# Kernel optimization log

Measured on AMD Instinct MI355X. Metric: run time of the kernel, lower is better.

The kernel has to match this reference:

```python
import jax, jax.numpy as jnp
import numpy as np
import math

N = 4096
BATCH = 8192


def _bitrev_perm(n):
    stages = int(math.log2(n))
    idx = np.arange(n, dtype=np.int64)
    rev = np.zeros(n, dtype=np.int64)
    v = idx.copy()
    for _ in range(stages):
        rev = (rev << 1) | (v & 1)
        v >>= 1
    return rev


def setup_inputs() -> dict:
    key = jax.random.key(0)
    k1, k2 = jax.random.split(key)
    x_re = jax.random.normal(k1, (BATCH, N), dtype=jnp.float32)
    x_im = jax.random.normal(k2, (BATCH, N), dtype=jnp.float32)
    k = np.arange(N, dtype=np.float32)
    angles = -2.0 * np.pi * k / N
    W_re = jnp.asarray(np.cos(angles), dtype=jnp.float32)
    W_im = jnp.asarray(np.sin(angles), dtype=jnp.float32)
    bitrev = jnp.asarray(_bitrev_perm(N))
    return {"x_re": x_re, "x_im": x_im, "W_re": W_re, "W_im": W_im, "bitrev": bitrev}


def reference(x_re, x_im, W_re, W_im, bitrev):
    n = x_re.shape[-1]
    num_stages = int(math.log2(n))
    # bit-reversal input permutation (the "wiring")
    y_re = x_re[..., bitrev]
    y_im = x_im[..., bitrev]
    for stage in range(num_stages):
        stride = 1 << stage
        group_size = stride << 1
        num_groups = n // group_size
        # (..., num_groups, group_size)
        y_re = y_re.reshape(*y_re.shape[:-1], num_groups, group_size)
        y_im = y_im.reshape(*y_im.shape[:-1], num_groups, group_size)
        upper_re = y_re[..., :stride]
        upper_im = y_im[..., :stride]
        lower_re = y_re[..., stride:]
        lower_im = y_im[..., stride:]
        tw_step = n // group_size
        tw_idx = jnp.arange(stride) * tw_step
        Wr = W_re[tw_idx]
        Wi = W_im[tw_idx]
        # complex twiddle multiply: W * lower
        wb_re = Wr * lower_re - Wi * lower_im
        wb_im = Wr * lower_im + Wi * lower_re
        y_re = jnp.concatenate([upper_re + wb_re, upper_re - wb_re], axis=-1)
        y_im = jnp.concatenate([upper_im + wb_im, upper_im - wb_im], axis=-1)
        y_re = y_re.reshape(*y_re.shape[:-2], n)
        y_im = y_im.reshape(*y_im.shape[:-2], n)
    return (y_re, y_im)
```

## Files before the change

kernel.cpp:

```cpp
#include <hip/hip_runtime.h>

#define FFT_N   4096
#define THREADS 512

__device__ __forceinline__ float2 cmul(float2 w, float2 v) {
    return make_float2(fmaf(w.x, v.x, -w.y * v.y), fmaf(w.x, v.y, w.y * v.x));
}
__device__ __forceinline__ float2 cmni(float2 v) { return make_float2(v.y, -v.x); }
__device__ __forceinline__ void bfly(float2& a, float2& b, float2 w) {
    float2 t = cmul(w, b);
    b = make_float2(a.x - t.x, a.y - t.y);
    a = make_float2(a.x + t.x, a.y + t.y);
}
__device__ __forceinline__ int swz(int i) { return i ^ ((i >> 4) & 15) ^ ((i >> 8) & 15); }

__device__ __forceinline__ void bar() {
    asm volatile("s_waitcnt lgkmcnt(0)" ::: "memory");
    __builtin_amdgcn_s_barrier();
}

__device__ __forceinline__ void radix8(float2 u[8], float2 A, float2 B, float2 C, float2 D) {
    bfly(u[0], u[1], A); bfly(u[2], u[3], A); bfly(u[4], u[5], A); bfly(u[6], u[7], A);
    float2 Bn = cmni(B);
    bfly(u[0], u[2], B); bfly(u[1], u[3], Bn); bfly(u[4], u[6], B); bfly(u[5], u[7], Bn);
    float2 Cn = cmni(C), Dn = cmni(D);
    bfly(u[0], u[4], C); bfly(u[1], u[5], D); bfly(u[2], u[6], Cn); bfly(u[3], u[7], Dn);
}

__device__ __forceinline__ void load_row(float2 u[8], const float* __restrict__ xr,
                                         const float* __restrict__ xi, int t) {
    u[0] = make_float2(xr[t],        xi[t]);
    u[1] = make_float2(xr[t + 2048], xi[t + 2048]);
    u[2] = make_float2(xr[t + 1024], xi[t + 1024]);
    u[3] = make_float2(xr[t + 3072], xi[t + 3072]);
    u[4] = make_float2(xr[t + 512],  xi[t + 512]);
    u[5] = make_float2(xr[t + 2560], xi[t + 2560]);
    u[6] = make_float2(xr[t + 1536], xi[t + 1536]);
    u[7] = make_float2(xr[t + 3584], xi[t + 3584]);
}

__device__ __forceinline__ void process_row(float2 u[8], float2* lds, int t,
        float2 C1, float2 C2, float2 C3, float2 w512,
        float* __restrict__ yr, float* __restrict__ yi)
{
    const float2 one = make_float2(1.f, 0.f);
    radix8(u, one, one, one, w512);
    const int g0 = (int)(__brev((unsigned)t) >> 23);
#pragma unroll
    for (int j = 0; j < 8; ++j) lds[swz(8 * g0 + j)] = u[j];
    bar();

    const int b1 = (t & 7) | (((t >> 4) & 1) << 6) | (((t >> 3) & 1) << 7) | ((t >> 5) << 8);
#pragma unroll
    for (int j = 0; j < 8; ++j) u[j] = lds[swz(b1 + 8 * j)];
    {
        float2 B = cmul(C1, C1), A = cmul(B, B), D = cmul(C1, w512);
        radix8(u, A, B, C1, D);
    }
#pragma unroll
    for (int j = 0; j < 8; ++j) lds[swz(b1 + 8 * j)] = u[j];
    bar();

    const int b2 = (t & 63) | ((t >> 6) << 9);
#pragma unroll
    for (int j = 0; j < 8; ++j) u[j] = lds[swz(b2 + 64 * j)];
    {
        float2 B = cmul(C2, C2), A = cmul(B, B), D = cmul(C2, w512);
        radix8(u, A, B, C2, D);
    }
#pragma unroll
    for (int j = 0; j < 8; ++j) lds[swz(b2 + 64 * j)] = u[j];
    bar();

#pragma unroll
    for (int j = 0; j < 8; ++j) u[j] = lds[swz(t + 512 * j)];
    {
        float2 B = cmul(C3, C3), A = cmul(B, B), D = cmul(C3, w512);
        radix8(u, A, B, C3, D);
    }
#pragma unroll
    for (int j = 0; j < 8; ++j) { yr[t + 512 * j] = u[j].x; yi[t + 512 * j] = u[j].y; }
    bar();
}

__global__ __launch_bounds__(THREADS) void fft4096_pipe_kernel(
    const float* __restrict__ x_re, const float* __restrict__ x_im,
    const float* __restrict__ W_re, const float* __restrict__ W_im,
    float* __restrict__ out, int batch, int rows_per)
{
    __shared__ float2 lds[FFT_N];
    const int t = threadIdx.x;

    const float2 C1 = make_float2(W_re[(t & 7) << 6],  W_im[(t & 7) << 6]);
    const float2 C2 = make_float2(W_re[(t & 63) << 3], W_im[(t & 63) << 3]);
    const float2 C3 = make_float2(W_re[t],             W_im[t]);
    const float2 w512 = make_float2(0.70710678118654752f, -0.70710678118654752f);

    const int row0 = blockIdx.x * rows_per;
    float2 ua[8], ub[8];

    if (rows_per & 1) {
        for (int i = 0; i < rows_per; ++i) {
            const int r = row0 + i;
            load_row(ua, x_re + (size_t)r * FFT_N, x_im + (size_t)r * FFT_N, t);
            process_row(ua, lds, t, C1, C2, C3, w512,
                        out + (size_t)r * FFT_N, out + ((size_t)batch + r) * FFT_N);
        }
        return;
    }

    load_row(ua, x_re + (size_t)row0 * FFT_N, x_im + (size_t)row0 * FFT_N, t);
    for (int i = 0; i < rows_per; i += 2) {
        const int ra = row0 + i, rb = ra + 1;
        load_row(ub, x_re + (size_t)rb * FFT_N, x_im + (size_t)rb * FFT_N, t);
        process_row(ua, lds, t, C1, C2, C3, w512,
                    out + (size_t)ra * FFT_N, out + ((size_t)batch + ra) * FFT_N);
        if (i + 2 < rows_per) {
            const int rc = ra + 2;
            load_row(ua, x_re + (size_t)rc * FFT_N, x_im + (size_t)rc * FFT_N, t);
        }
        process_row(ub, lds, t, C1, C2, C3, w512,
                    out + (size_t)rb * FFT_N, out + ((size_t)batch + rb) * FFT_N);
    }
}

extern "C" void kernel_launch(void* const* d_in, const int* in_sizes, int n_in,
                              void* d_out, int out_size, void* d_ws, size_t ws_size,
                              hipStream_t stream) {
    const float* x_re = (const float*)d_in[0];
    const float* x_im = (const float*)d_in[1];
    const float* W_re = (const float*)d_in[2];
    const float* W_im = (const float*)d_in[3];
    const int batch = in_sizes[0] / FFT_N;
    float* out = (float*)d_out;

    int rows_per = 8;
    while (rows_per > 1 && (batch % rows_per)) rows_per >>= 1;
    const int grid = batch / rows_per;
    fft4096_pipe_kernel<<<grid, THREADS, 0, stream>>>(x_re, x_im, W_re, W_im, out, batch, rows_per);
}
```

Baseline: 112.8 us.

## Halve threads and process two interleaved sub-FFTs per thread with float4 LDS

Each thread now handles 16 complex points, two interleaved columns, instead of 8. This halves the block to 256 threads, lets global loads and stores be float2-vectorized, and packs LDS traffic into float4 with a new XOR swizzle. Output stores use nontemporal hints. The goal is fewer memory instructions and wider accesses, in exchange for higher register pressure, which the launch_bounds occupancy hint of 4 blocks tries to contain.

```diff
diff --git a/kernel.cpp b/kernel.cpp
--- a/kernel.cpp
+++ b/kernel.cpp
@@ -1,7 +1,7 @@
 #include <hip/hip_runtime.h>
 
 #define FFT_N   4096
-#define THREADS 512
+#define THREADS 256
 
 __device__ __forceinline__ float2 cmul(float2 w, float2 v) {
     return make_float2(fmaf(w.x, v.x, -w.y * v.y), fmaf(w.x, v.y, w.y * v.x));
@@ -12,13 +12,13 @@
     b = make_float2(a.x - t.x, a.y - t.y);
     a = make_float2(a.x + t.x, a.y + t.y);
 }
-__device__ __forceinline__ int swz(int i) { return i ^ ((i >> 4) & 15) ^ ((i >> 8) & 15); }
-
+__device__ __forceinline__ int sslot(int p) {
+    return p ^ ((p >> 3) & 7) ^ ((p >> 6) & 7) ^ ((p >> 9) & 7);
+}
 __device__ __forceinline__ void bar() {
     asm volatile("s_waitcnt lgkmcnt(0)" ::: "memory");
     __builtin_amdgcn_s_barrier();
 }
-
 __device__ __forceinline__ void radix8(float2 u[8], float2 A, float2 B, float2 C, float2 D) {
     bfly(u[0], u[1], A); bfly(u[2], u[3], A); bfly(u[4], u[5], A); bfly(u[6], u[7], A);
     float2 Bn = cmni(B);
@@ -27,100 +27,131 @@
     bfly(u[0], u[4], C); bfly(u[1], u[5], D); bfly(u[2], u[6], Cn); bfly(u[3], u[7], Dn);
 }
 
-__device__ __forceinline__ void load_row(float2 u[8], const float* __restrict__ xr,
-                                         const float* __restrict__ xi, int t) {
-    u[0] = make_float2(xr[t],        xi[t]);
-    u[1] = make_float2(xr[t + 2048], xi[t + 2048]);
-    u[2] = make_float2(xr[t + 1024], xi[t + 1024]);
-    u[3] = make_float2(xr[t + 3072], xi[t + 3072]);
-    u[4] = make_float2(xr[t + 512],  xi[t + 512]);
-    u[5] = make_float2(xr[t + 2560], xi[t + 2560]);
-    u[6] = make_float2(xr[t + 1536], xi[t + 1536]);
-    u[7] = make_float2(xr[t + 3584], xi[t + 3584]);
+__device__ __forceinline__ void nt_store_f2(float* p, float2 v) {
+    union { float2 f; unsigned long long u; } cv; cv.f = v;
+    __builtin_nontemporal_store(cv.u, (unsigned long long*)p);
 }
 
-__device__ __forceinline__ void process_row(float2 u[8], float2* lds, int t,
-        float2 C1, float2 C2, float2 C3, float2 w512,
+struct RowBuf { float2 re[8]; float2 im[8]; };
+
+__device__ __forceinline__ void load_row(RowBuf& rb, const float* __restrict__ xr,
+                                         const float* __restrict__ xi, int t2) {
+    const int off[8] = {0, 2048, 1024, 3072, 512, 2560, 1536, 3584};
+#pragma unroll
+    for (int j = 0; j < 8; ++j) {
+        rb.re[j] = *(const float2*)(xr + t2 + off[j]);
+        rb.im[j] = *(const float2*)(xi + t2 + off[j]);
+    }
+}
+
+__device__ __forceinline__ void process_row(const RowBuf& rb, float4* lds, int t,
+        float2 C1, float2 C2, float2 C3u, float2 C3v,
         float* __restrict__ yr, float* __restrict__ yi)
 {
-    const float2 one = make_float2(1.f, 0.f);
+    const float2 one  = make_float2(1.f, 0.f);
+    const float2 w512 = make_float2(0.70710678118654752f, -0.70710678118654752f);
+    float2 u[8], v[8];
+
+#pragma unroll
+    for (int j = 0; j < 8; ++j) {
+        u[j] = make_float2(rb.re[j].x, rb.im[j].x);
+        v[j] = make_float2(rb.re[j].y, rb.im[j].y);
+    }
     radix8(u, one, one, one, w512);
-    const int g0 = (int)(__brev((unsigned)t) >> 23);
+    radix8(v, one, one, one, w512);
+    const int g = (int)(__brev((unsigned)t) >> 24);
 #pragma unroll
-    for (int j = 0; j < 8; ++j) lds[swz(8 * g0 + j)] = u[j];
+    for (int j = 0; j < 8; ++j)
+        lds[sslot(8 * g + j)] = make_float4(u[j].x, u[j].y, v[j].x, v[j].y);
     bar();
 
-    const int b1 = (t & 7) | (((t >> 4) & 1) << 6) | (((t >> 3) & 1) << 7) | ((t >> 5) << 8);
+    const int a1 = (t & 7) | ((t >> 3) << 6);
 #pragma unroll
-    for (int j = 0; j < 8; ++j) u[j] = lds[swz(b1 + 8 * j)];
-    {
-        float2 B = cmul(C1, C1), A = cmul(B, B), D = cmul(C1, w512);
-        radix8(u, A, B, C1, D);
+    for (int j = 0; j < 8; ++j) {
+        float4 f = lds[sslot(a1 + 8 * j)];
+        u[j] = make_float2(f.x, f.y); v[j] = make_float2(f.z, f.w);
     }
+    { float2 B = cmul(C1, C1), A = cmul(B, B), D = cmul(C1, w512);
+      radix8(u, A, B, C1, D); radix8(v, A, B, C1, D); }
 #pragma unroll
-    for (int j = 0; j < 8; ++j) lds[swz(b1 + 8 * j)] = u[j];
+    for (int j = 0; j < 8; ++j)
+        lds[sslot(a1 + 8 * j)] = make_float4(u[j].x, u[j].y, v[j].x, v[j].y);
     bar();
 
-    const int b2 = (t & 63) | ((t >> 6) << 9);
+    const int a2 = (t & 63) | ((t >> 6) << 9);
 #pragma unroll
-    for (int j = 0; j < 8; ++j) u[j] = lds[swz(b2 + 64 * j)];
-    {
-        float2 B = cmul(C2, C2), A = cmul(B, B), D = cmul(C2, w512);
-        radix8(u, A, B, C2, D);
+    for (int j = 0; j < 8; ++j) {
+        float4 f = lds[sslot(a2 + 64 * j)];
+        u[j] = make_float2(f.x, f.y); v[j] = make_float2(f.z, f.w);
     }
+    { float2 B = cmul(C2, C2), A = cmul(B, B), D = cmul(C2, w512);
+      radix8(u, A, B, C2, D); radix8(v, A, B, C2, D); }
 #pragma unroll
-    for (int j = 0; j < 8; ++j) lds[swz(b2 + 64 * j)] = u[j];
+    for (int j = 0; j < 8; ++j)
+        lds[sslot(a2 + 64 * j)] = make_float4(u[j].x, u[j].y, v[j].x, v[j].y);
     bar();
 
+    const int c = 2 * t;
 #pragma unroll
-    for (int j = 0; j < 8; ++j) u[j] = lds[swz(t + 512 * j)];
-    {
-        float2 B = cmul(C3, C3), A = cmul(B, B), D = cmul(C3, w512);
-        radix8(u, A, B, C3, D);
+    for (int j = 0; j < 4; ++j) {
+        float4 f0 = lds[sslot(c + 512 * j)];
+        float4 f1 = lds[sslot(c + 1 + 512 * j)];
+        u[j] = make_float2(f0.x, f0.y); u[j + 4] = make_float2(f0.z, f0.w);
+        v[j] = make_float2(f1.x, f1.y); v[j + 4] = make_float2(f1.z, f1.w);
     }
+    { float2 B = cmul(C3u, C3u), A = cmul(B, B), D = cmul(C3u, w512);
+      radix8(u, A, B, C3u, D); }
+    { float2 B = cmul(C3v, C3v), A = cmul(B, B), D = cmul(C3v, w512);
+      radix8(v, A, B, C3v, D); }
 #pragma unroll
-    for (int j = 0; j < 8; ++j) { yr[t + 512 * j] = u[j].x; yi[t + 512 * j] = u[j].y; }
+    for (int j = 0; j < 8; ++j) {
+        nt_store_f2(yr + c + 512 * j, make_float2(u[j].x, v[j].x));
+        nt_store_f2(yi + c + 512 * j, make_float2(u[j].y, v[j].y));
+    }
     bar();
 }
 
-__global__ __launch_bounds__(THREADS) void fft4096_pipe_kernel(
+__global__ __launch_bounds__(THREADS, 4) void fft4096_p2_kernel(
     const float* __restrict__ x_re, const float* __restrict__ x_im,
     const float* __restrict__ W_re, const float* __restrict__ W_im,
     float* __restrict__ out, int batch, int rows_per)
 {
-    __shared__ float2 lds[FFT_N];
+    __shared__ float4 lds[FFT_N / 2];
     const int t = threadIdx.x;
 
     const float2 C1 = make_float2(W_re[(t & 7) << 6],  W_im[(t & 7) << 6]);
     const float2 C2 = make_float2(W_re[(t & 63) << 3], W_im[(t & 63) << 3]);
-    const float2 C3 = make_float2(W_re[t],             W_im[t]);
-    const float2 w512 = make_float2(0.70710678118654752f, -0.70710678118654752f);
+    const float2 wr2 = ((const float2*)W_re)[t];
+    const float2 wi2 = ((const float2*)W_im)[t];
+    const float2 C3u = make_float2(wr2.x, wi2.x);
+    const float2 C3v = make_float2(wr2.y, wi2.y);
 
+    const int t2 = 2 * t;
     const int row0 = blockIdx.x * rows_per;
-    float2 ua[8], ub[8];
+    RowBuf ra, rb;
 
     if (rows_per & 1) {
         for (int i = 0; i < rows_per; ++i) {
             const int r = row0 + i;
-            load_row(ua, x_re + (size_t)r * FFT_N, x_im + (size_t)r * FFT_N, t);
-            process_row(ua, lds, t, C1, C2, C3, w512,
+            load_row(ra, x_re + (size_t)r * FFT_N, x_im + (size_t)r * FFT_N, t2);
+            process_row(ra, lds, t, C1, C2, C3u, C3v,
                         out + (size_t)r * FFT_N, out + ((size_t)batch + r) * FFT_N);
         }
         return;
     }
 
-    load_row(ua, x_re + (size_t)row0 * FFT_N, x_im + (size_t)row0 * FFT_N, t);
+    load_row(ra, x_re + (size_t)row0 * FFT_N, x_im + (size_t)row0 * FFT_N, t2);
     for (int i = 0; i < rows_per; i += 2) {
-        const int ra = row0 + i, rb = ra + 1;
-        load_row(ub, x_re + (size_t)rb * FFT_N, x_im + (size_t)rb * FFT_N, t);
-        process_row(ua, lds, t, C1, C2, C3, w512,
-                    out + (size_t)ra * FFT_N, out + ((size_t)batch + ra) * FFT_N);
+        const int r0 = row0 + i, r1 = r0 + 1;
+        load_row(rb, x_re + (size_t)r1 * FFT_N, x_im + (size_t)r1 * FFT_N, t2);
+        process_row(ra, lds, t, C1, C2, C3u, C3v,
+                    out + (size_t)r0 * FFT_N, out + ((size_t)batch + r0) * FFT_N);
         if (i + 2 < rows_per) {
-            const int rc = ra + 2;
-            load_row(ua, x_re + (size_t)rc * FFT_N, x_im + (size_t)rc * FFT_N, t);
+            const int r2 = r0 + 2;
+            load_row(ra, x_re + (size_t)r2 * FFT_N, x_im + (size_t)r2 * FFT_N, t2);
         }
-        process_row(ub, lds, t, C1, C2, C3, w512,
-                    out + (size_t)rb * FFT_N, out + ((size_t)batch + rb) * FFT_N);
+        process_row(rb, lds, t, C1, C2, C3u, C3v,
+                    out + (size_t)r1 * FFT_N, out + ((size_t)batch + r1) * FFT_N);
     }
 }
 
@@ -137,5 +168,5 @@
     int rows_per = 8;
     while (rows_per > 1 && (batch % rows_per)) rows_per >>= 1;
     const int grid = batch / rows_per;
-    fft4096_pipe_kernel<<<grid, THREADS, 0, stream>>>(x_re, x_im, W_re, W_im, out, batch, rows_per);
+    fft4096_p2_kernel<<<grid, THREADS, 0, stream>>>(x_re, x_im, W_re, W_im, out, batch, rows_per);
 }
```

New measurement: 329.6 us. 192% more time.

## Switch 4096-point FFT from four radix-8 passes to three radix-16 passes

Applied to the files above, without the earlier changes.

Replaces the four radix-8 stages, which need three LDS exchanges and barriers, with three radix-16 stages that need two exchanges, using 256 threads holding 16 elements each. The first stage uses specialized trivial-twiddle butterflies. The explicit two-row register double-buffering of global loads is dropped in favour of a simple per-row loop. This cuts LDS traffic and barriers but raises register pressure and lowers threads per block, which may hurt latency hiding.

```diff
diff --git a/kernel.cpp b/kernel.cpp
--- a/kernel.cpp
+++ b/kernel.cpp
@@ -1,7 +1,7 @@
 #include <hip/hip_runtime.h>
 
 #define FFT_N   4096
-#define THREADS 512
+#define THREADS 256
 
 __device__ __forceinline__ float2 cmul(float2 w, float2 v) {
     return make_float2(fmaf(w.x, v.x, -w.y * v.y), fmaf(w.x, v.y, w.y * v.x));
@@ -12,78 +12,79 @@
     b = make_float2(a.x - t.x, a.y - t.y);
     a = make_float2(a.x + t.x, a.y + t.y);
 }
+__device__ __forceinline__ void bfly1(float2& a, float2& b) {
+    float2 t = b;
+    b = make_float2(a.x - t.x, a.y - t.y);
+    a = make_float2(a.x + t.x, a.y + t.y);
+}
+__device__ __forceinline__ void bflyni(float2& a, float2& b) {
+    float2 t = make_float2(b.y, -b.x);
+    b = make_float2(a.x - t.x, a.y - t.y);
+    a = make_float2(a.x + t.x, a.y + t.y);
+}
 __device__ __forceinline__ int swz(int i) { return i ^ ((i >> 4) & 15) ^ ((i >> 8) & 15); }
-
 __device__ __forceinline__ void bar() {
     asm volatile("s_waitcnt lgkmcnt(0)" ::: "memory");
     __builtin_amdgcn_s_barrier();
 }
 
-__device__ __forceinline__ void radix8(float2 u[8], float2 A, float2 B, float2 C, float2 D) {
-    bfly(u[0], u[1], A); bfly(u[2], u[3], A); bfly(u[4], u[5], A); bfly(u[6], u[7], A);
-    float2 Bn = cmni(B);
-    bfly(u[0], u[2], B); bfly(u[1], u[3], Bn); bfly(u[4], u[6], B); bfly(u[5], u[7], Bn);
-    float2 Cn = cmni(C), Dn = cmni(D);
-    bfly(u[0], u[4], C); bfly(u[1], u[5], D); bfly(u[2], u[6], Cn); bfly(u[3], u[7], Dn);
+#define Q1x  0.70710678118654752f
+#define Q3x -0.70710678118654752f
+#define E1x 0.923879532511286756f
+#define E1y -0.382683432365089772f
+#define E3x 0.382683432365089772f
+#define E3y -0.923879532511286756f
+
+__device__ __forceinline__ void radix16(float2 u[16], float2 G, float2 G2, float2 G4, float2 G8) {
+#pragma unroll
+    for (int m = 0; m < 16; m += 2) bfly(u[m], u[m + 1], G8);
+    float2 G4n = cmni(G4);
+#pragma unroll
+    for (int b = 0; b < 16; b += 4) { bfly(u[b], u[b + 2], G4); bfly(u[b + 1], u[b + 3], G4n); }
+    float2 t1 = cmul(G2, make_float2(Q1x, -Q1x));
+    float2 t2 = cmni(G2);
+    float2 t3 = cmul(G2, make_float2(Q3x, -Q1x));
+#pragma unroll
+    for (int b = 0; b < 16; b += 8) {
+        bfly(u[b + 0], u[b + 4], G2); bfly(u[b + 1], u[b + 5], t1);
+        bfly(u[b + 2], u[b + 6], t2); bfly(u[b + 3], u[b + 7], t3);
+    }
+    float2 s1 = cmul(G, make_float2(E1x, E1y));
+    float2 s2 = cmul(G, make_float2(Q1x, -Q1x));
+    float2 s3 = cmul(G, make_float2(E3x, E3y));
+    float2 s4 = cmni(G);
+    float2 s5 = cmni(s1);
+    float2 s6 = cmni(s2);
+    float2 s7 = cmni(s3);
+    bfly(u[0], u[8],  G);  bfly(u[1], u[9],  s1);
+    bfly(u[2], u[10], s2); bfly(u[3], u[11], s3);
+    bfly(u[4], u[12], s4); bfly(u[5], u[13], s5);
+    bfly(u[6], u[14], s6); bfly(u[7], u[15], s7);
 }
 
-__device__ __forceinline__ void load_row(float2 u[8], const float* __restrict__ xr,
-                                         const float* __restrict__ xi, int t) {
-    u[0] = make_float2(xr[t],        xi[t]);
-    u[1] = make_float2(xr[t + 2048], xi[t + 2048]);
-    u[2] = make_float2(xr[t + 1024], xi[t + 1024]);
-    u[3] = make_float2(xr[t + 3072], xi[t + 3072]);
-    u[4] = make_float2(xr[t + 512],  xi[t + 512]);
-    u[5] = make_float2(xr[t + 2560], xi[t + 2560]);
-    u[6] = make_float2(xr[t + 1536], xi[t + 1536]);
-    u[7] = make_float2(xr[t + 3584], xi[t + 3584]);
+__device__ __forceinline__ void radix16_first(float2 u[16]) {
+#pragma unroll
+    for (int m = 0; m < 16; m += 2) bfly1(u[m], u[m + 1]);
+#pragma unroll
+    for (int b = 0; b < 16; b += 4) { bfly1(u[b], u[b + 2]); bflyni(u[b + 1], u[b + 3]); }
+#pragma unroll
+    for (int b = 0; b < 16; b += 8) {
+        bfly1(u[b + 0], u[b + 4]);
+        bfly(u[b + 1], u[b + 5], make_float2(Q1x, -Q1x));
+        bflyni(u[b + 2], u[b + 6]);
+        bfly(u[b + 3], u[b + 7], make_float2(Q3x, -Q1x));
+    }
+    bfly1(u[0], u[8]);
+    bfly(u[1], u[9],  make_float2(E1x, E1y));
+    bfly(u[2], u[10], make_float2(Q1x, -Q1x));
+    bfly(u[3], u[11], make_float2(E3x, E3y));
+    bflyni(u[4], u[12]);
+    bfly(u[5], u[13], make_float2(E1y, -E1x));
+    bfly(u[6], u[14], make_float2(Q3x, -Q1x));
+    bfly(u[7], u[15], make_float2(E3y, -E3x));
 }
 
-__device__ __forceinline__ void process_row(float2 u[8], float2* lds, int t,
-        float2 C1, float2 C2, float2 C3, float2 w512,
-        float* __restrict__ yr, float* __restrict__ yi)
-{
-    const float2 one = make_float2(1.f, 0.f);
-    radix8(u, one, one, one, w512);
-    const int g0 = (int)(__brev((unsigned)t) >> 23);
-#pragma unroll
-    for (int j = 0; j < 8; ++j) lds[swz(8 * g0 + j)] = u[j];
-    bar();
-
-    const int b1 = (t & 7) | (((t >> 4) & 1) << 6) | (((t >> 3) & 1) << 7) | ((t >> 5) << 8);
-#pragma unroll
-    for (int j = 0; j < 8; ++j) u[j] = lds[swz(b1 + 8 * j)];
-    {
-        float2 B = cmul(C1, C1), A = cmul(B, B), D = cmul(C1, w512);
-        radix8(u, A, B, C1, D);
-    }
-#pragma unroll
-    for (int j = 0; j < 8; ++j) lds[swz(b1 + 8 * j)] = u[j];
-    bar();
-
-    const int b2 = (t & 63) | ((t >> 6) << 9);
-#pragma unroll
-    for (int j = 0; j < 8; ++j) u[j] = lds[swz(b2 + 64 * j)];
-    {
-        float2 B = cmul(C2, C2), A = cmul(B, B), D = cmul(C2, w512);
-        radix8(u, A, B, C2, D);
-    }
-#pragma unroll
-    for (int j = 0; j < 8; ++j) lds[swz(b2 + 64 * j)] = u[j];
-    bar();
-
-#pragma unroll
-    for (int j = 0; j < 8; ++j) u[j] = lds[swz(t + 512 * j)];
-    {
-        float2 B = cmul(C3, C3), A = cmul(B, B), D = cmul(C3, w512);
-        radix8(u, A, B, C3, D);
-    }
-#pragma unroll
-    for (int j = 0; j < 8; ++j) { yr[t + 512 * j] = u[j].x; yi[t + 512 * j] = u[j].y; }
-    bar();
-}
-
-__global__ __launch_bounds__(THREADS) void fft4096_pipe_kernel(
+__global__ __launch_bounds__(THREADS) void fft4096_r16_kernel(
     const float* __restrict__ x_re, const float* __restrict__ x_im,
     const float* __restrict__ W_re, const float* __restrict__ W_im,
     float* __restrict__ out, int batch, int rows_per)
@@ -91,36 +92,52 @@
     __shared__ float2 lds[FFT_N];
     const int t = threadIdx.x;
 
-    const float2 C1 = make_float2(W_re[(t & 7) << 6],  W_im[(t & 7) << 6]);
-    const float2 C2 = make_float2(W_re[(t & 63) << 3], W_im[(t & 63) << 3]);
-    const float2 C3 = make_float2(W_re[t],             W_im[t]);
-    const float2 w512 = make_float2(0.70710678118654752f, -0.70710678118654752f);
+    const int rB = t & 15;
+    const float2 GB  = make_float2(W_re[rB << 4], W_im[rB << 4]);
+    const float2 GB2 = cmul(GB, GB);
+    const float2 GB4 = cmul(GB2, GB2);
+    const float2 GB8 = cmul(GB4, GB4);
+    const float2 GC  = make_float2(W_re[t], W_im[t]);
+    const float2 GC2 = cmul(GC, GC);
+    const float2 GC4 = cmul(GC2, GC2);
+    const float2 GC8 = cmul(GC4, GC4);
 
+    const int g  = (int)(__brev((unsigned)t) >> 24);
+    const int bB = (t & 15) | ((t >> 4) << 8);
     const int row0 = blockIdx.x * rows_per;
-    float2 ua[8], ub[8];
+    float* out_im = out + (size_t)batch * FFT_N;
 
-    if (rows_per & 1) {
-        for (int i = 0; i < rows_per; ++i) {
-            const int r = row0 + i;
-            load_row(ua, x_re + (size_t)r * FFT_N, x_im + (size_t)r * FFT_N, t);
-            process_row(ua, lds, t, C1, C2, C3, w512,
-                        out + (size_t)r * FFT_N, out + ((size_t)batch + r) * FFT_N);
-        }
-        return;
-    }
+    for (int i = 0; i < rows_per; ++i) {
+        const int r = row0 + i;
+        const float* xr = x_re + (size_t)r * FFT_N;
+        const float* xi = x_im + (size_t)r * FFT_N;
+        float2 u[16];
 
-    load_row(ua, x_re + (size_t)row0 * FFT_N, x_im + (size_t)row0 * FFT_N, t);
-    for (int i = 0; i < rows_per; i += 2) {
-        const int ra = row0 + i, rb = ra + 1;
-        load_row(ub, x_re + (size_t)rb * FFT_N, x_im + (size_t)rb * FFT_N, t);
-        process_row(ua, lds, t, C1, C2, C3, w512,
-                    out + (size_t)ra * FFT_N, out + ((size_t)batch + ra) * FFT_N);
-        if (i + 2 < rows_per) {
-            const int rc = ra + 2;
-            load_row(ua, x_re + (size_t)rc * FFT_N, x_im + (size_t)rc * FFT_N, t);
-        }
-        process_row(ub, lds, t, C1, C2, C3, w512,
-                    out + (size_t)rb * FFT_N, out + ((size_t)batch + rb) * FFT_N);
+        const int off[16] = {0, 2048, 1024, 3072, 512, 2560, 1536, 3584,
+                             256, 2304, 1280, 3328, 768, 2816, 1792, 3840};
+#pragma unroll
+        for (int j = 0; j < 16; ++j) u[j] = make_float2(xr[t + off[j]], xi[t + off[j]]);
+
+        radix16_first(u);
+#pragma unroll
+        for (int j = 0; j < 16; ++j) lds[swz(16 * g + j)] = u[j];
+        bar();
+
+#pragma unroll
+        for (int j = 0; j < 16; ++j) u[j] = lds[swz(bB + 16 * j)];
+        radix16(u, GB, GB2, GB4, GB8);
+#pragma unroll
+        for (int j = 0; j < 16; ++j) lds[swz(bB + 16 * j)] = u[j];
+        bar();
+
+#pragma unroll
+        for (int j = 0; j < 16; ++j) u[j] = lds[swz(t + 256 * j)];
+        radix16(u, GC, GC2, GC4, GC8);
+        float* yr = out + (size_t)r * FFT_N;
+        float* yi = out_im + (size_t)r * FFT_N;
+#pragma unroll
+        for (int j = 0; j < 16; ++j) { yr[t + 256 * j] = u[j].x; yi[t + 256 * j] = u[j].y; }
+        bar();
     }
 }
 
@@ -137,5 +154,5 @@
     int rows_per = 8;
     while (rows_per > 1 && (batch % rows_per)) rows_per >>= 1;
     const int grid = batch / rows_per;
-    fft4096_pipe_kernel<<<grid, THREADS, 0, stream>>>(x_re, x_im, W_re, W_im, out, batch, rows_per);
+    fft4096_r16_kernel<<<grid, THREADS, 0, stream>>>(x_re, x_im, W_re, W_im, out, batch, rows_per);
 }
```

Measured after the change: 123.6 us. 9.6% more time.
